# Optimization experiments

Measured on AMD Instinct MI355X. Metric: run time of the kernel, lower is better.

The kernel has to match this reference:

```python
import jax, jax.numpy as jnp
import numpy as np

EMBED_DIM = 1536
BOTTLENECK = 64
EPS = 1e-5  # torch LayerNorm default


def setup_inputs() -> dict:
    key = jax.random.key(0)
    ks = jax.random.split(key, 6)
    x = jax.random.normal(ks[0], (32768, EMBED_DIM), dtype=jnp.float32)
    # Xavier-uniform init for down (matches nn.init.xavier_uniform_)
    limit = float(np.sqrt(6.0 / (EMBED_DIM + BOTTLENECK)))
    w_down = jax.random.uniform(ks[1], (BOTTLENECK, EMBED_DIM), jnp.float32, -limit, limit)
    b_down = jnp.zeros((BOTTLENECK,), jnp.float32)
    # Torch initializes up to zeros; use small random values so gradients/outputs are non-trivial
    w_up = jax.random.normal(ks[2], (EMBED_DIM, BOTTLENECK), dtype=jnp.float32) * 0.02
    b_up = jnp.zeros((EMBED_DIM,), jnp.float32)
    gamma = jnp.ones((EMBED_DIM,), jnp.float32)
    beta = jnp.zeros((EMBED_DIM,), jnp.float32)
    return {"x": x, "w_down": w_down, "b_down": b_down, "w_up": w_up,
            "b_up": b_up, "gamma": gamma, "beta": beta}


def reference(x, w_down, b_down, w_up, b_up, gamma, beta):
    residual = x
    # LayerNorm over last dim
    mean = jnp.mean(x, axis=-1, keepdims=True)
    var = jnp.mean(jnp.square(x - mean), axis=-1, keepdims=True)
    h = (x - mean) * jax.lax.rsqrt(var + EPS) * gamma + beta
    # down-proj -> exact GELU -> (dropout=identity at inference) -> up-proj
    h = jnp.einsum('nd,bd->nb', h, w_down) + b_down  # [N, 64]
    h = jax.nn.gelu(h, approximate=False)            # torch F.gelu default (erf)
    h = jnp.einsum('nb,db->nd', h, w_up) + b_up      # [N, 1536]
    out = residual + h
    # F.normalize(p=2, dim=-1) with eps=1e-12
    norm = jnp.maximum(jnp.linalg.norm(out, axis=-1, keepdims=True), 1e-12)
    return out / norm
```

## Files before the change

### kernel.cpp

```cpp
#include <hip/hip_runtime.h>
#include <math.h>

#define EMBED 1536
#define BN 64
#define XS_STRIDE 1544
#define GS_STRIDE 80

typedef __attribute__((ext_vector_type(8))) short short8;
typedef __attribute__((ext_vector_type(4))) float f32x4;

__device__ inline unsigned short f2bf(float f) {
    union { float f; unsigned u; } c; c.f = f;
    unsigned u = c.u;
    return (unsigned short)((u + 0x7fffu + ((u >> 16) & 1u)) >> 16);
}
__device__ inline float bf2f(unsigned short h) {
    union { unsigned u; float f; } c; c.u = ((unsigned)h) << 16;
    return c.f;
}

__global__ void prep_kernel(const float* __restrict__ w_down, const float* __restrict__ w_up,
                            const float* __restrict__ gamma, const float* __restrict__ beta,
                            unsigned short* __restrict__ wdg, unsigned short* __restrict__ wub,
                            float* __restrict__ c1, float* __restrict__ c2) {
    int blk = blockIdx.x;
    if (blk < 384) {
        int i = blk * 256 + threadIdx.x;
        int d = i % EMBED;
        wdg[i] = f2bf(w_down[i] * gamma[d]);
        wub[i] = f2bf(w_up[i]);
        return;
    }
    int b = blk - 384;
    int t = threadIdx.x;
    float s1 = 0.f, s2 = 0.f;
    for (int d = t; d < EMBED; d += 256) {
        float w = w_down[b * EMBED + d];
        s1 += gamma[d] * w;
        s2 += beta[d] * w;
    }
    #pragma unroll
    for (int m = 1; m < 64; m <<= 1) { s1 += __shfl_xor(s1, m); s2 += __shfl_xor(s2, m); }
    __shared__ float r1[4], r2[4];
    int wave = t >> 6, lane = t & 63;
    if (lane == 0) { r1[wave] = s1; r2[wave] = s2; }
    __syncthreads();
    if (t == 0) {
        c1[b] = r1[0] + r1[1] + r1[2] + r1[3];
        c2[b] = r2[0] + r2[1] + r2[2] + r2[3];
    }
}

__global__ __launch_bounds__(256, 3) void fused_kernel(
    const float* __restrict__ x, const float* __restrict__ b_down,
    const float* __restrict__ b_up,
    const unsigned short* __restrict__ wdg, const unsigned short* __restrict__ wub,
    const float* __restrict__ c1, const float* __restrict__ c2,
    float* __restrict__ out)
{
    __shared__ unsigned short xs[16 * XS_STRIDE];
    __shared__ unsigned short gs[16 * GS_STRIDE];
    __shared__ float mean_s[16], rstd_s[16], sumsq_s[16], inv_s[16];

    const int tid  = threadIdx.x;
    const int wave = tid >> 6, lane = tid & 63;
    const int l16  = lane & 15, quad = lane >> 4;
    const long row0 = (long)blockIdx.x * 16;

    {
        float4 v[4][6];
        #pragma unroll
        for (int j = 0; j < 4; ++j) {
            const float4* xp = (const float4*)(x + (row0 + wave * 4 + j) * EMBED);
            #pragma unroll
            for (int k = 0; k < 6; ++k) v[j][k] = xp[lane + 64 * k];
        }
        #pragma unroll
        for (int j = 0; j < 4; ++j) {
            int lr = wave * 4 + j;
            float s = 0.f, ss = 0.f;
            #pragma unroll
            for (int k = 0; k < 6; ++k) {
                s  += v[j][k].x + v[j][k].y + v[j][k].z + v[j][k].w;
                ss += v[j][k].x * v[j][k].x + v[j][k].y * v[j][k].y
                    + v[j][k].z * v[j][k].z + v[j][k].w * v[j][k].w;
            }
            #pragma unroll
            for (int m = 1; m < 64; m <<= 1) { s += __shfl_xor(s, m); ss += __shfl_xor(ss, m); }
            float mean = s * (1.f / EMBED);
            float var  = ss * (1.f / EMBED) - mean * mean;
            if (lane == 0) {
                mean_s[lr] = mean;
                rstd_s[lr] = rsqrtf(var + 1e-5f);
                sumsq_s[lr] = 0.f;
            }
            #pragma unroll
            for (int k = 0; k < 6; ++k) {
                ushort4 p;
                p.x = f2bf(v[j][k].x); p.y = f2bf(v[j][k].y);
                p.z = f2bf(v[j][k].z); p.w = f2bf(v[j][k].w);
                *(ushort4*)(&xs[lr * XS_STRIDE + 4 * (lane + 64 * k)]) = p;
            }
        }
    }
    __syncthreads();

    f32x4 acc = {0.f, 0.f, 0.f, 0.f};
    {
        const unsigned short* arow = &xs[l16 * XS_STRIDE];
        const unsigned short* brow = wdg + (size_t)(wave * 16 + l16) * EMBED;
        #pragma unroll 4
        for (int kk = 0; kk < 48; ++kk) {
            int ko = kk * 32 + quad * 8;
            short8 a = *(const short8*)(arow + ko);
            short8 b = *(const short8*)(brow + ko);
            acc = __builtin_amdgcn_mfma_f32_16x16x32_bf16(a, b, acc, 0, 0, 0);
        }
    }
    {
        int bg = wave * 16 + l16;
        float c1v = c1[bg], c2v = c2[bg], bdv = b_down[bg];
        #pragma unroll
        for (int reg = 0; reg < 4; ++reg) {
            int r = quad * 4 + reg;
            float rs = rstd_s[r];
            float v = rs * acc[reg] - rs * mean_s[r] * c1v + c2v + bdv;
            float g = 0.5f * v * (1.f + erff(v * 0.70710678118654752f));
            gs[r * GS_STRIDE + bg] = f2bf(g);
        }
    }
    __syncthreads();

    short8 gb0 = *(const short8*)(&gs[l16 * GS_STRIDE + quad * 8]);
    short8 gb1 = *(const short8*)(&gs[l16 * GS_STRIDE + 32 + quad * 8]);
    const int dbase = wave * 384;
    f32x4 cc[24];
    float sqs = 0.f;
    #pragma unroll
    for (int t = 0; t < 24; ++t) {
        int d0 = dbase + t * 16;
        int dm = d0 + quad * 4;
        float4 bu = *(const float4*)(b_up + dm);
        ushort4 rx = *(const ushort4*)(&xs[l16 * XS_STRIDE + dm]);
        f32x4 c;
        c[0] = bf2f(rx.x) + bu.x;
        c[1] = bf2f(rx.y) + bu.y;
        c[2] = bf2f(rx.z) + bu.z;
        c[3] = bf2f(rx.w) + bu.w;
        const unsigned short* wrow = wub + (size_t)(d0 + l16) * 64;
        short8 a0 = *(const short8*)(wrow + quad * 8);
        short8 a1 = *(const short8*)(wrow + 32 + quad * 8);
        c = __builtin_amdgcn_mfma_f32_16x16x32_bf16(a0, gb0, c, 0, 0, 0);
        c = __builtin_amdgcn_mfma_f32_16x16x32_bf16(a1, gb1, c, 0, 0, 0);
        cc[t] = c;
        sqs += c[0] * c[0] + c[1] * c[1] + c[2] * c[2] + c[3] * c[3];
    }
    sqs += __shfl_xor(sqs, 16);
    sqs += __shfl_xor(sqs, 32);
    if (lane < 16) atomicAdd(&sumsq_s[l16], sqs);
    __syncthreads();
    if (tid < 16) inv_s[tid] = 1.f / fmaxf(sqrtf(sumsq_s[tid]), 1e-12f);
    __syncthreads();

    const float inv = inv_s[l16];
    float* orow = out + (row0 + l16) * EMBED;
    #pragma unroll
    for (int t = 0; t < 24; ++t) {
        int dm = dbase + t * 16 + quad * 4;
        f32x4 c = cc[t];
        float4 o;
        o.x = c[0] * inv; o.y = c[1] * inv; o.z = c[2] * inv; o.w = c[3] * inv;
        *(float4*)(orow + dm) = o;
    }
}

extern "C" void kernel_launch(void* const* d_in, const int* in_sizes, int n_in,
                              void* d_out, int out_size, void* d_ws, size_t ws_size,
                              hipStream_t stream)
{
    const float* x      = (const float*)d_in[0];
    const float* w_down = (const float*)d_in[1];
    const float* b_down = (const float*)d_in[2];
    const float* w_up   = (const float*)d_in[3];
    const float* b_up   = (const float*)d_in[4];
    const float* gamma  = (const float*)d_in[5];
    const float* beta   = (const float*)d_in[6];
    float* out = (float*)d_out;

    const int N = in_sizes[0] / EMBED;

    unsigned short* wdg = (unsigned short*)d_ws;
    unsigned short* wub = wdg + BN * EMBED;
    float* c1 = (float*)(wub + BN * EMBED);
    float* c2 = c1 + BN;

    prep_kernel<<<384 + BN, 256, 0, stream>>>(w_down, w_up, gamma, beta, wdg, wub, c1, c2);
    fused_kernel<<<N / 16, 256, 0, stream>>>(x, b_down, b_up, wdg, wub, c1, c2, out);
}
```

Before: 421.7 us.

## Drop LDS staging of x and fuse LayerNorm statistics into the down-projection loop

Removes the shared-memory bf16 copy of the 16-row x tile. Each wave now loads x directly from global memory as fp32 inside the down-projection MFMA loop, converting to bf16 on the fly and accumulating row sum and sum of squares there. The residual is re-read from global memory in fp32, and the final normalisation barrier is folded away. This cuts LDS traffic, a barrier and the LDS footprint, but all four waves now read the same rows, x is read twice per block, and the per-lane access pattern is strided across rows, so it leans on the cache. Launch bounds are relaxed to one block.

```diff
diff --git a/kernel.cpp b/kernel.cpp
--- a/kernel.cpp
+++ b/kernel.cpp
@@ -3,7 +3,6 @@
 
 #define EMBED 1536
 #define BN 64
-#define XS_STRIDE 1544
 #define GS_STRIDE 80
 
 typedef __attribute__((ext_vector_type(8))) short short8;
@@ -13,10 +12,6 @@
     union { float f; unsigned u; } c; c.f = f;
     unsigned u = c.u;
     return (unsigned short)((u + 0x7fffu + ((u >> 16) & 1u)) >> 16);
-}
-__device__ inline float bf2f(unsigned short h) {
-    union { unsigned u; float f; } c; c.u = ((unsigned)h) << 16;
-    return c.f;
 }
 
 __global__ void prep_kernel(const float* __restrict__ w_down, const float* __restrict__ w_up,
@@ -51,81 +46,60 @@
     }
 }
 
-__global__ __launch_bounds__(256, 3) void fused_kernel(
+__global__ __launch_bounds__(256, 1) void fused_kernel(
     const float* __restrict__ x, const float* __restrict__ b_down,
     const float* __restrict__ b_up,
     const unsigned short* __restrict__ wdg, const unsigned short* __restrict__ wub,
     const float* __restrict__ c1, const float* __restrict__ c2,
     float* __restrict__ out)
 {
-    __shared__ unsigned short xs[16 * XS_STRIDE];
     __shared__ unsigned short gs[16 * GS_STRIDE];
-    __shared__ float mean_s[16], rstd_s[16], sumsq_s[16], inv_s[16];
+    __shared__ float sumsq_s[16];
 
     const int tid  = threadIdx.x;
     const int wave = tid >> 6, lane = tid & 63;
     const int l16  = lane & 15, quad = lane >> 4;
     const long row0 = (long)blockIdx.x * 16;
+    const float* xrow = x + (row0 + l16) * EMBED;
 
-    {
-        float4 v[4][6];
-        #pragma unroll
-        for (int j = 0; j < 4; ++j) {
-            const float4* xp = (const float4*)(x + (row0 + wave * 4 + j) * EMBED);
-            #pragma unroll
-            for (int k = 0; k < 6; ++k) v[j][k] = xp[lane + 64 * k];
-        }
-        #pragma unroll
-        for (int j = 0; j < 4; ++j) {
-            int lr = wave * 4 + j;
-            float s = 0.f, ss = 0.f;
-            #pragma unroll
-            for (int k = 0; k < 6; ++k) {
-                s  += v[j][k].x + v[j][k].y + v[j][k].z + v[j][k].w;
-                ss += v[j][k].x * v[j][k].x + v[j][k].y * v[j][k].y
-                    + v[j][k].z * v[j][k].z + v[j][k].w * v[j][k].w;
-            }
-            #pragma unroll
-            for (int m = 1; m < 64; m <<= 1) { s += __shfl_xor(s, m); ss += __shfl_xor(ss, m); }
-            float mean = s * (1.f / EMBED);
-            float var  = ss * (1.f / EMBED) - mean * mean;
-            if (lane == 0) {
-                mean_s[lr] = mean;
-                rstd_s[lr] = rsqrtf(var + 1e-5f);
-                sumsq_s[lr] = 0.f;
-            }
-            #pragma unroll
-            for (int k = 0; k < 6; ++k) {
-                ushort4 p;
-                p.x = f2bf(v[j][k].x); p.y = f2bf(v[j][k].y);
-                p.z = f2bf(v[j][k].z); p.w = f2bf(v[j][k].w);
-                *(ushort4*)(&xs[lr * XS_STRIDE + 4 * (lane + 64 * k)]) = p;
-            }
-        }
-    }
-    __syncthreads();
+    if (tid < 16) sumsq_s[tid] = 0.f;
 
     f32x4 acc = {0.f, 0.f, 0.f, 0.f};
+    float s = 0.f, ss = 0.f;
     {
-        const unsigned short* arow = &xs[l16 * XS_STRIDE];
         const unsigned short* brow = wdg + (size_t)(wave * 16 + l16) * EMBED;
         #pragma unroll 4
         for (int kk = 0; kk < 48; ++kk) {
             int ko = kk * 32 + quad * 8;
-            short8 a = *(const short8*)(arow + ko);
+            float4 a0 = *(const float4*)(xrow + ko);
+            float4 a1 = *(const float4*)(xrow + ko + 4);
             short8 b = *(const short8*)(brow + ko);
-            acc = __builtin_amdgcn_mfma_f32_16x16x32_bf16(a, b, acc, 0, 0, 0);
+            s  += (a0.x + a0.y) + (a0.z + a0.w) + (a1.x + a1.y) + (a1.z + a1.w);
+            ss += a0.x * a0.x + a0.y * a0.y + a0.z * a0.z + a0.w * a0.w
+                + a1.x * a1.x + a1.y * a1.y + a1.z * a1.z + a1.w * a1.w;
+            short8 af;
+            af[0] = (short)f2bf(a0.x); af[1] = (short)f2bf(a0.y);
+            af[2] = (short)f2bf(a0.z); af[3] = (short)f2bf(a0.w);
+            af[4] = (short)f2bf(a1.x); af[5] = (short)f2bf(a1.y);
+            af[6] = (short)f2bf(a1.z); af[7] = (short)f2bf(a1.w);
+            acc = __builtin_amdgcn_mfma_f32_16x16x32_bf16(af, b, acc, 0, 0, 0);
         }
     }
+    s  += __shfl_xor(s, 16);  s  += __shfl_xor(s, 32);
+    ss += __shfl_xor(ss, 16); ss += __shfl_xor(ss, 32);
+    float mean = s * (1.f / EMBED);
+    float rstd = rsqrtf(ss * (1.f / EMBED) - mean * mean + 1e-5f);
+    float rsm  = rstd * mean;
     {
         int bg = wave * 16 + l16;
         float c1v = c1[bg], c2v = c2[bg], bdv = b_down[bg];
         #pragma unroll
         for (int reg = 0; reg < 4; ++reg) {
             int r = quad * 4 + reg;
-            float rs = rstd_s[r];
-            float v = rs * acc[reg] - rs * mean_s[r] * c1v + c2v + bdv;
-            float g = 0.5f * v * (1.f + erff(v * 0.70710678118654752f));
+            float rs = __shfl(rstd, r);
+            float rm = __shfl(rsm, r);
+            float vv = rs * acc[reg] - rm * c1v + c2v + bdv;
+            float g = 0.5f * vv * (1.f + erff(vv * 0.70710678118654752f));
             gs[r * GS_STRIDE + bg] = f2bf(g);
         }
     }
@@ -141,12 +115,12 @@
         int d0 = dbase + t * 16;
         int dm = d0 + quad * 4;
         float4 bu = *(const float4*)(b_up + dm);
-        ushort4 rx = *(const ushort4*)(&xs[l16 * XS_STRIDE + dm]);
+        float4 rx = *(const float4*)(xrow + dm);
         f32x4 c;
-        c[0] = bf2f(rx.x) + bu.x;
-        c[1] = bf2f(rx.y) + bu.y;
-        c[2] = bf2f(rx.z) + bu.z;
-        c[3] = bf2f(rx.w) + bu.w;
+        c[0] = rx.x + bu.x;
+        c[1] = rx.y + bu.y;
+        c[2] = rx.z + bu.z;
+        c[3] = rx.w + bu.w;
         const unsigned short* wrow = wub + (size_t)(d0 + l16) * 64;
         short8 a0 = *(const short8*)(wrow + quad * 8);
         short8 a1 = *(const short8*)(wrow + 32 + quad * 8);
@@ -159,10 +133,8 @@
     sqs += __shfl_xor(sqs, 32);
     if (lane < 16) atomicAdd(&sumsq_s[l16], sqs);
     __syncthreads();
-    if (tid < 16) inv_s[tid] = 1.f / fmaxf(sqrtf(sumsq_s[tid]), 1e-12f);
-    __syncthreads();
 
-    const float inv = inv_s[l16];
+    const float inv = 1.f / fmaxf(sqrtf(sumsq_s[l16]), 1e-12f);
     float* orow = out + (row0 + l16) * EMBED;
     #pragma unroll
     for (int t = 0; t < 24; ++t) {
```

Result: slower. 524.2 us (+24.3%).
